# Kernel tuning notes

Hardware: AMD Instinct MI355X
Metric: run time of the kernel (lower is better)

The kernel has to match this reference:

```python
import jax, jax.numpy as jnp
import numpy as np

NPOINT, NSAMPLE, RADIUS, EPS = 128, 32, 0.4, 1e-5
C_IN, C_MID, C_OUT = 256, 256, 256


def setup_inputs() -> dict:
    key = jax.random.key(0)
    ks = jax.random.split(key, 6)
    B, N = 8, 16384
    xyz = jax.random.uniform(ks[0], (B, N, 3), dtype=jnp.float32)
    feats = jax.random.normal(ks[1], (B, N, C_IN), dtype=jnp.float32)
    # SharedMLP: Conv2d 1x1 (no bias, followed by BN) layers 259->256, 256->256
    w1 = jax.random.normal(ks[2], (C_MID, C_IN + 3), dtype=jnp.float32) * 0.05
    w2 = jax.random.normal(ks[3], (C_OUT, C_MID), dtype=jnp.float32) * 0.05
    gamma1 = jnp.ones((C_MID,), jnp.float32); beta1 = jnp.zeros((C_MID,), jnp.float32)
    mean1 = jnp.zeros((C_MID,), jnp.float32); var1 = jnp.ones((C_MID,), jnp.float32)
    gamma2 = jnp.ones((C_OUT,), jnp.float32); beta2 = jnp.zeros((C_OUT,), jnp.float32)
    mean2 = jnp.zeros((C_OUT,), jnp.float32); var2 = jnp.ones((C_OUT,), jnp.float32)
    return {"xyz": xyz, "proposal_features": feats,
            "w1": w1, "gamma1": gamma1, "beta1": beta1, "mean1": mean1, "var1": var1,
            "w2": w2, "gamma2": gamma2, "beta2": beta2, "mean2": mean2, "var2": var2}


def fps(xyz, npoint):
    # Farthest point sampling, CUDA-kernel-faithful: starts at index 0.
    B, N, _ = xyz.shape
    def step(carry, _):
        dist, far = carry
        centroid = jnp.take_along_axis(xyz, far[:, None, None], axis=1)  # [B,1,3]
        d = jnp.sum((xyz - centroid) ** 2, axis=-1)                      # [B,N]
        dist = jnp.minimum(dist, d)
        return (dist, jnp.argmax(dist, axis=-1).astype(jnp.int32)), far
    init = (jnp.full((B, N), 1e10, xyz.dtype), jnp.zeros((B,), jnp.int32))
    _, inds = jax.lax.scan(step, init, None, length=npoint)
    return inds.T  # [B, npoint]


def ball_query(xyz, new_xyz, radius, nsample):
    # First-nsample-in-order points within radius, padded with the first hit.
    B, N, _ = xyz.shape
    d2 = jnp.sum((new_xyz[:, :, None, :] - xyz[:, None, :, :]) ** 2, axis=-1)  # [B,S,N]
    keys = jnp.where(d2 < radius * radius, jnp.arange(N, dtype=jnp.int32), N)
    idx = -jax.lax.top_k(-keys, nsample)[0]  # smallest indices, ascending
    idx = jnp.where(idx < N, idx, idx[..., :1])  # pad invalid with first hit
    return jnp.clip(idx, 0, N - 1)


def gather_points(pts_bnc, idx):
    # pts_bnc [B,N,C], idx [B,S,K] -> [B,S,K,C]
    B, S, K = idx.shape
    flat = jnp.take_along_axis(pts_bnc, idx.reshape(B, S * K)[:, :, None], axis=1)
    return flat.reshape(B, S, K, pts_bnc.shape[-1])


def bn_relu(x, gamma, beta, mean, var):
    return jax.nn.relu((x - mean) * jax.lax.rsqrt(var + EPS) * gamma + beta)


def reference(xyz, proposal_features, w1, gamma1, beta1, mean1, var1,
              w2, gamma2, beta2, mean2, var2):
    # proposal_features arrives as [B, N, C]; torch module permutes to [B, C, N]
    # (we keep channels-last internally, equivalent math).
    inds = fps(xyz, NPOINT)                                   # [B,128]
    new_xyz = jnp.take_along_axis(xyz, inds[:, :, None], axis=1)  # [B,128,3]
    idx = ball_query(xyz, new_xyz, RADIUS, NSAMPLE)           # [B,128,32]
    g_xyz = gather_points(xyz, idx) - new_xyz[:, :, None, :]  # [B,128,32,3]
    g_feat = gather_points(proposal_features, idx)            # [B,128,32,256]
    x = jnp.concatenate([g_xyz, g_feat], axis=-1)             # [B,128,32,259]
    h = bn_relu(jnp.einsum('bskc,oc->bsko', x, w1), gamma1, beta1, mean1, var1)
    h = bn_relu(jnp.einsum('bskc,oc->bsko', h, w2), gamma2, beta2, mean2, var2)
    new_features = jnp.max(h, axis=2)                         # [B,128,256]
    return jnp.transpose(new_features, (0, 2, 1))             # [B,256,128]
```

## Files before the change

### kernel.cpp

```cpp
#include <hip/hip_runtime.h>
#include <hip/hip_bf16.h>
#include <cstdint>
#include <cstddef>

#define NB      8
#define NPTS    16384
#define NPOINT  128
#define NSAMPLE 32
#define CIN     256
#define CMID    256
#define COUT    256
#define KDIM    259
#define KPAD    288
#define XS_STRIDE 296
#define HS_STRIDE 264

typedef __attribute__((ext_vector_type(8))) short bf16x8;
typedef __attribute__((ext_vector_type(4))) float f32x4;
typedef __attribute__((ext_vector_type(2))) float f32x2;

__device__ __forceinline__ short f2bf(float f) {
  unsigned u = __float_as_uint(f);
  u += 0x7fffu + ((u >> 16) & 1u);
  return (short)(u >> 16);
}

template <int CTRL, int RMASK>
__device__ __forceinline__ unsigned long long dpp_umax_step(unsigned long long v) {
  int lo = (int)(unsigned)(v & 0xffffffffull);
  int hi = (int)(unsigned)(v >> 32);
  int nlo = __builtin_amdgcn_update_dpp(lo, lo, CTRL, RMASK, 0xf, false);
  int nhi = __builtin_amdgcn_update_dpp(hi, hi, CTRL, RMASK, 0xf, false);
  unsigned long long o = ((unsigned long long)(unsigned)nhi << 32) | (unsigned)nlo;
  return o > v ? o : v;
}

#define FPS_T 512
#define FPS_W (FPS_T / 64)
#define FPS_P (NPTS / FPS_T)
#define FPS_PH (FPS_P / 2)

__global__ __launch_bounds__(FPS_T) __attribute__((amdgpu_waves_per_eu(2, 2)))
void fps_kernel(const float* __restrict__ xyz, int* __restrict__ inds) {
#pragma clang fp contract(off)
  const int b = blockIdx.x;
  const int t = threadIdx.x;
  const int lane = t & 63, w = t >> 6;
  const float* xb = xyz + (size_t)b * NPTS * 3;

  f32x2 px[FPS_PH], py[FPS_PH], pz[FPS_PH], dv[FPS_PH];
#pragma unroll
  for (int i = 0; i < FPS_PH; ++i) {
    const int j0 = t + (2 * i) * FPS_T;
    const int j1 = j0 + FPS_T;
    px[i] = (f32x2){xb[j0 * 3 + 0], xb[j1 * 3 + 0]};
    py[i] = (f32x2){xb[j0 * 3 + 1], xb[j1 * 3 + 1]};
    pz[i] = (f32x2){xb[j0 * 3 + 2], xb[j1 * 3 + 2]};
    dv[i] = (f32x2){1e10f, 1e10f};
  }
#pragma unroll
  for (int i = 0; i < FPS_PH; ++i) {
    asm volatile("" : "+v"(px[i]), "+v"(py[i]), "+v"(pz[i]), "+v"(dv[i]));
  }

  __shared__ unsigned long long s_pack[2][FPS_W];
  __shared__ float swx[2][FPS_W], swy[2][FPS_W], swz[2][FPS_W];

  int far = 0;
  float cx = xb[0], cy = xb[1], cz = xb[2];

  for (int it = 0; it < NPOINT; ++it) {
    if (t == 0) inds[b * NPOINT + it] = far;
    const f32x2 vcx = {cx, cx}, vcy = {cy, cy}, vcz = {cz, cz};
    f32x2 best2 = {-1.0f, -1.0f};
#pragma unroll
    for (int i = 0; i < FPS_PH; ++i) {
      f32x2 dx = px[i] - vcx;
      f32x2 dy = py[i] - vcy;
      f32x2 dz = pz[i] - vcz;
      f32x2 d2 = (dx * dx + dy * dy) + dz * dz;
      f32x2 dm = {fminf(dv[i].x, d2.x), fminf(dv[i].y, d2.y)};
      dv[i] = dm;
      best2 = (f32x2){fmaxf(best2.x, dm.x), fmaxf(best2.y, dm.y)};
    }
    const float best = fmaxf(best2.x, best2.y);
    int sl = 0;
#pragma unroll
    for (int i = FPS_PH - 1; i >= 0; --i) {
      if (dv[i].y == best) sl = 2 * i + 1;
      if (dv[i].x == best) sl = 2 * i;
    }
    const int bi = t + (sl << 9);

    unsigned long long pk = ((unsigned long long)__float_as_uint(best) << 17)
                          | ((unsigned long long)(unsigned)(NPTS - 1 - bi) << 3)
                          | (unsigned long long)w;

    pk = dpp_umax_step<0x111, 0xf>(pk);
    pk = dpp_umax_step<0x112, 0xf>(pk);
    pk = dpp_umax_step<0x114, 0xf>(pk);
    pk = dpp_umax_step<0x118, 0xf>(pk);
    pk = dpp_umax_step<0x142, 0xa>(pk);
    pk = dpp_umax_step<0x143, 0xc>(pk);
    const unsigned wlo = (unsigned)__builtin_amdgcn_readlane((int)(unsigned)(pk & 0xffffffffull), 63);
    const unsigned whi = (unsigned)__builtin_amdgcn_readlane((int)(unsigned)(pk >> 32), 63);
    const unsigned long long wavepk = ((unsigned long long)whi << 32) | wlo;
    const int wbi = (NPTS - 1) - (int)((wavepk >> 3) & (unsigned long long)(NPTS - 1));

    const int slot = __builtin_amdgcn_readfirstlane(wbi >> 9);
    float bx = 0.f, by = 0.f, bz = 0.f;
#define CASE_SLOT(k) \
    case (2 * (k)):     bx = px[k].x; by = py[k].x; bz = pz[k].x; break; \
    case (2 * (k) + 1): bx = px[k].y; by = py[k].y; bz = pz[k].y; break;
    switch (slot) {
      CASE_SLOT(0)  CASE_SLOT(1)  CASE_SLOT(2)  CASE_SLOT(3)
      CASE_SLOT(4)  CASE_SLOT(5)  CASE_SLOT(6)  CASE_SLOT(7)
      CASE_SLOT(8)  CASE_SLOT(9)  CASE_SLOT(10) CASE_SLOT(11)
      CASE_SLOT(12) CASE_SLOT(13) CASE_SLOT(14) CASE_SLOT(15)
      default: break;
    }
#undef CASE_SLOT

    const int par = it & 1;
    if (lane == (wbi & 63)) {
      s_pack[par][w] = wavepk;
      swx[par][w] = bx; swy[par][w] = by; swz[par][w] = bz;
    }
    __syncthreads();
    unsigned long long pm = s_pack[par][lane & 7];
    pm = dpp_umax_step<0x124, 0xf>(pm);
    pm = dpp_umax_step<0x4E, 0xf>(pm);
    pm = dpp_umax_step<0xB1, 0xf>(pm);
    const int wi = (int)(pm & 7ull);
    far = (NPTS - 1) - (int)((pm >> 3) & (unsigned long long)(NPTS - 1));
    cx = swx[par][wi]; cy = swy[par][wi]; cz = swz[par][wi];
  }
}

__global__ __launch_bounds__(256) void ballq_kernel(const float* __restrict__ xyz,
                                                    const int* __restrict__ inds,
                                                    int* __restrict__ idx) {
  const int gw   = (blockIdx.x * 256 + threadIdx.x) >> 6;
  const int lane = threadIdx.x & 63;
  const int b = gw >> 7, s = gw & 127;
  const float* xb = xyz + (size_t)b * NPTS * 3;
  const int ind = inds[b * NPOINT + s];
  const float cx = xb[ind * 3 + 0], cy = xb[ind * 3 + 1], cz = xb[ind * 3 + 2];
  int* o = idx + gw * NSAMPLE;
  const float R2 = (float)(0.4 * 0.4);
  int total = 0;
  int first_hit = 0;
  bool have_first = false;
  for (int base = 0; base < NPTS && total < NSAMPLE; base += 64) {
    const int j = base + lane;
    float dx = __fsub_rn(xb[j * 3 + 0], cx);
    float dy = __fsub_rn(xb[j * 3 + 1], cy);
    float dz = __fsub_rn(xb[j * 3 + 2], cz);
    float d2 = __fadd_rn(__fadd_rn(__fmul_rn(dx, dx), __fmul_rn(dy, dy)), __fmul_rn(dz, dz));
    bool hit = d2 < R2;
    unsigned long long m = __ballot(hit);
    if (!have_first && m) { first_hit = base + (int)__builtin_ctzll(m); have_first = true; }
    int pos = total + (int)__popcll(m & ((1ull << lane) - 1ull));
    if (hit && pos < NSAMPLE) o[pos] = j;
    total += (int)__popcll(m);
  }
  for (int p = total + lane; p < NSAMPLE; p += 64) o[p] = first_hit;
}

__global__ __launch_bounds__(256) void prep_kernel(
    const float* __restrict__ w1, const float* __restrict__ g1, const float* __restrict__ be1,
    const float* __restrict__ m1, const float* __restrict__ v1,
    const float* __restrict__ w2, const float* __restrict__ g2, const float* __restrict__ be2,
    const float* __restrict__ m2, const float* __restrict__ v2,
    short* __restrict__ w1b, short* __restrict__ w2b,
    float* __restrict__ b1, float* __restrict__ b2) {
  int i = blockIdx.x * 256 + threadIdx.x;
  if (i < CMID * KPAD) {
    int oc = i / KPAD, c = i - oc * KPAD;
    float a = g1[oc] * rsqrtf(v1[oc] + 1e-5f);
    float val = (c < KDIM) ? w1[oc * KDIM + c] * a : 0.0f;
    w1b[i] = f2bf(val);
    if (c == 0) b1[oc] = be1[oc] - m1[oc] * a;
  }
  if (i < COUT * CMID) {
    int oc = i >> 8, c = i & 255;
    float a = g2[oc] * rsqrtf(v2[oc] + 1e-5f);
    w2b[i] = f2bf(w2[oc * CMID + c] * a);
    if (c == 0) b2[oc] = be2[oc] - m2[oc] * a;
  }
}

__global__ __launch_bounds__(256) void mlp_kernel(
    const float* __restrict__ xyz, const float* __restrict__ feats,
    const int* __restrict__ inds, const int* __restrict__ idx,
    const short* __restrict__ w1b, const short* __restrict__ w2b,
    const float* __restrict__ b1, const float* __restrict__ b2,
    float* __restrict__ out) {
  const int g   = blockIdx.x;
  const int bb  = g >> 7, s = g & 127;
  const int tid = threadIdx.x;
  const int wave = tid >> 6, lane = tid & 63;
  const int lrow = lane & 15, quad = lane >> 4;

  __shared__ short Xs[32 * XS_STRIDE];
  __shared__ short Hs[32 * HS_STRIDE];
  __shared__ int   sj[NSAMPLE];
  __shared__ float scen[3];

  if (tid < NSAMPLE) sj[tid] = idx[g * NSAMPLE + tid];
  if (tid < 3) {
    int ind = inds[bb * NPOINT + s];
    scen[tid] = xyz[((size_t)bb * NPTS + ind) * 3 + tid];
  }
  __syncthreads();

  for (int e = tid; e < 32 * KPAD; e += 256) {
    int r = e / KPAD, c = e - r * KPAD;
    int j = sj[r];
    float val;
    if (c < 3)          val = xyz[((size_t)bb * NPTS + j) * 3 + c] - scen[c];
    else if (c < KDIM)  val = feats[((size_t)bb * NPTS + j) * CIN + (c - 3)];
    else                val = 0.0f;
    Xs[r * XS_STRIDE + c] = f2bf(val);
  }
  __syncthreads();

  const int nw = wave * 64;
  f32x4 acc[4][2];
#pragma unroll
  for (int nt = 0; nt < 4; ++nt)
#pragma unroll
    for (int mt = 0; mt < 2; ++mt) acc[nt][mt] = (f32x4){0.f, 0.f, 0.f, 0.f};

  for (int ks = 0; ks < 9; ++ks) {
    const int ko = ks * 32 + quad * 8;
    bf16x8 a0 = *(const bf16x8*)(&Xs[lrow * XS_STRIDE + ko]);
    bf16x8 a1 = *(const bf16x8*)(&Xs[(lrow + 16) * XS_STRIDE + ko]);
#pragma unroll
    for (int nt = 0; nt < 4; ++nt) {
      const int oc = nw + nt * 16 + lrow;
      bf16x8 bf = *(const bf16x8*)(w1b + oc * KPAD + ko);
      acc[nt][0] = __builtin_amdgcn_mfma_f32_16x16x32_bf16(a0, bf, acc[nt][0], 0, 0, 0);
      acc[nt][1] = __builtin_amdgcn_mfma_f32_16x16x32_bf16(a1, bf, acc[nt][1], 0, 0, 0);
    }
  }

#pragma unroll
  for (int nt = 0; nt < 4; ++nt) {
    const int oc = nw + nt * 16 + lrow;
    const float bias = b1[oc];
#pragma unroll
    for (int mt = 0; mt < 2; ++mt) {
#pragma unroll
      for (int r = 0; r < 4; ++r) {
        int row = mt * 16 + quad * 4 + r;
        float h = fmaxf(acc[nt][mt][r] + bias, 0.0f);
        Hs[row * HS_STRIDE + oc] = f2bf(h);
      }
    }
  }
  __syncthreads();

#pragma unroll
  for (int nt = 0; nt < 4; ++nt)
#pragma unroll
    for (int mt = 0; mt < 2; ++mt) acc[nt][mt] = (f32x4){0.f, 0.f, 0.f, 0.f};

  for (int ks = 0; ks < 8; ++ks) {
    const int ko = ks * 32 + quad * 8;
    bf16x8 a0 = *(const bf16x8*)(&Hs[lrow * HS_STRIDE + ko]);
    bf16x8 a1 = *(const bf16x8*)(&Hs[(lrow + 16) * HS_STRIDE + ko]);
#pragma unroll
    for (int nt = 0; nt < 4; ++nt) {
      const int oc = nw + nt * 16 + lrow;
      bf16x8 bf = *(const bf16x8*)(w2b + oc * CMID + ko);
      acc[nt][0] = __builtin_amdgcn_mfma_f32_16x16x32_bf16(a0, bf, acc[nt][0], 0, 0, 0);
      acc[nt][1] = __builtin_amdgcn_mfma_f32_16x16x32_bf16(a1, bf, acc[nt][1], 0, 0, 0);
    }
  }

#pragma unroll
  for (int nt = 0; nt < 4; ++nt) {
    const int oc = nw + nt * 16 + lrow;
    const float bias = b2[oc];
    float v = -3.4e38f;
#pragma unroll
    for (int mt = 0; mt < 2; ++mt) {
      f32x4 a = acc[nt][mt];
      v = fmaxf(v, fmaxf(fmaxf(a[0], a[1]), fmaxf(a[2], a[3])));
    }
    v = fmaxf(v + bias, 0.0f);
    v = fmaxf(v, __shfl_xor(v, 16, 64));
    v = fmaxf(v, __shfl_xor(v, 32, 64));
    if (lane < 16) out[((size_t)bb * COUT + oc) * NPOINT + s] = v;
  }
}

extern "C" void kernel_launch(void* const* d_in, const int* in_sizes, int n_in,
                              void* d_out, int out_size, void* d_ws, size_t ws_size,
                              hipStream_t stream) {
  const float* xyz   = (const float*)d_in[0];
  const float* feats = (const float*)d_in[1];
  const float* w1    = (const float*)d_in[2];
  const float* g1    = (const float*)d_in[3];
  const float* be1   = (const float*)d_in[4];
  const float* m1    = (const float*)d_in[5];
  const float* v1    = (const float*)d_in[6];
  const float* w2    = (const float*)d_in[7];
  const float* g2    = (const float*)d_in[8];
  const float* be2   = (const float*)d_in[9];
  const float* m2    = (const float*)d_in[10];
  const float* v2    = (const float*)d_in[11];
  float* out = (float*)d_out;

  char* ws = (char*)d_ws;
  int*   inds = (int*)(ws);
  int*   idx  = (int*)(ws + 4096);
  short* w1b  = (short*)(ws + 135168);
  short* w2b  = (short*)(ws + 282624);
  float* b1   = (float*)(ws + 413696);
  float* b2   = (float*)(ws + 414720);

  prep_kernel<<<288, 256, 0, stream>>>(w1, g1, be1, m1, v1, w2, g2, be2, m2, v2,
                                       w1b, w2b, b1, b2);
  fps_kernel<<<NB, FPS_T, 0, stream>>>(xyz, inds);
  ballq_kernel<<<256, 256, 0, stream>>>(xyz, inds, idx);
  mlp_kernel<<<NB * NPOINT, 256, 0, stream>>>(xyz, feats, inds, idx, w1b, w2b, b1, b2, out);
}
```

Before: 456.4 us.

## Split farthest point sampling across four blocks per batch with global atomic sync

Each batch's farthest point sampling now runs on four workgroups, each owning a quarter of the points, so each thread holds fewer points and does less work per iteration. The per-block winners are merged every iteration through a global atomicMax on a packed distance/index key plus an arrival counter that the blocks spin on. The new centroid is then reloaded from global memory instead of being broadcast through shared memory. This adds a device-wide synchronisation round trip on each of the 128 iterations. The spin loop has a timeout, so correctness assumes all 32 workgroups are co-resident.

```diff
diff --git a/kernel.cpp b/kernel.cpp
--- a/kernel.cpp
+++ b/kernel.cpp
@@ -35,23 +35,30 @@
   return o > v ? o : v;
 }
 
-#define FPS_T 512
-#define FPS_W (FPS_T / 64)
-#define FPS_P (NPTS / FPS_T)
+#define FPS_K  4
+#define FPS_T  512
+#define FPS_W  (FPS_T / 64)
+#define FPS_PTS (NPTS / FPS_K)
+#define FPS_P  (FPS_PTS / FPS_T)
 #define FPS_PH (FPS_P / 2)
 
 __global__ __launch_bounds__(FPS_T) __attribute__((amdgpu_waves_per_eu(2, 2)))
-void fps_kernel(const float* __restrict__ xyz, int* __restrict__ inds) {
+void fps_kernel(const float* __restrict__ xyz, int* __restrict__ inds,
+                unsigned long long* __restrict__ slot, unsigned* __restrict__ cnt) {
 #pragma clang fp contract(off)
-  const int b = blockIdx.x;
+  const int bk = blockIdx.x;
+  const int b = bk >> 2, k = bk & 3;
   const int t = threadIdx.x;
   const int lane = t & 63, w = t >> 6;
   const float* xb = xyz + (size_t)b * NPTS * 3;
+  const int base = k * FPS_PTS;
+  unsigned long long* sl_b = slot + b * NPOINT;
+  unsigned* cn_b = cnt + b * NPOINT;
 
   f32x2 px[FPS_PH], py[FPS_PH], pz[FPS_PH], dv[FPS_PH];
 #pragma unroll
   for (int i = 0; i < FPS_PH; ++i) {
-    const int j0 = t + (2 * i) * FPS_T;
+    const int j0 = base + t + (2 * i) * FPS_T;
     const int j1 = j0 + FPS_T;
     px[i] = (f32x2){xb[j0 * 3 + 0], xb[j1 * 3 + 0]};
     py[i] = (f32x2){xb[j0 * 3 + 1], xb[j1 * 3 + 1]};
@@ -64,13 +71,12 @@
   }
 
   __shared__ unsigned long long s_pack[2][FPS_W];
-  __shared__ float swx[2][FPS_W], swy[2][FPS_W], swz[2][FPS_W];
 
   int far = 0;
   float cx = xb[0], cy = xb[1], cz = xb[2];
 
   for (int it = 0; it < NPOINT; ++it) {
-    if (t == 0) inds[b * NPOINT + it] = far;
+    if (k == 0 && t == 0) inds[b * NPOINT + it] = far;
     const f32x2 vcx = {cx, cx}, vcy = {cy, cy}, vcz = {cz, cz};
     f32x2 best2 = {-1.0f, -1.0f};
 #pragma unroll
@@ -90,11 +96,10 @@
       if (dv[i].y == best) sl = 2 * i + 1;
       if (dv[i].x == best) sl = 2 * i;
     }
-    const int bi = t + (sl << 9);
-
-    unsigned long long pk = ((unsigned long long)__float_as_uint(best) << 17)
-                          | ((unsigned long long)(unsigned)(NPTS - 1 - bi) << 3)
-                          | (unsigned long long)w;
+    const int bi = base + t + (sl << 9);
+
+    unsigned long long pk = ((unsigned long long)__float_as_uint(best) << 14)
+                          | (unsigned long long)(unsigned)(NPTS - 1 - bi);
 
     pk = dpp_umax_step<0x111, 0xf>(pk);
     pk = dpp_umax_step<0x112, 0xf>(pk);
@@ -105,35 +110,29 @@
     const unsigned wlo = (unsigned)__builtin_amdgcn_readlane((int)(unsigned)(pk & 0xffffffffull), 63);
     const unsigned whi = (unsigned)__builtin_amdgcn_readlane((int)(unsigned)(pk >> 32), 63);
     const unsigned long long wavepk = ((unsigned long long)whi << 32) | wlo;
-    const int wbi = (NPTS - 1) - (int)((wavepk >> 3) & (unsigned long long)(NPTS - 1));
-
-    const int slot = __builtin_amdgcn_readfirstlane(wbi >> 9);
-    float bx = 0.f, by = 0.f, bz = 0.f;
-#define CASE_SLOT(k) \
-    case (2 * (k)):     bx = px[k].x; by = py[k].x; bz = pz[k].x; break; \
-    case (2 * (k) + 1): bx = px[k].y; by = py[k].y; bz = pz[k].y; break;
-    switch (slot) {
-      CASE_SLOT(0)  CASE_SLOT(1)  CASE_SLOT(2)  CASE_SLOT(3)
-      CASE_SLOT(4)  CASE_SLOT(5)  CASE_SLOT(6)  CASE_SLOT(7)
-      CASE_SLOT(8)  CASE_SLOT(9)  CASE_SLOT(10) CASE_SLOT(11)
-      CASE_SLOT(12) CASE_SLOT(13) CASE_SLOT(14) CASE_SLOT(15)
-      default: break;
-    }
-#undef CASE_SLOT
 
     const int par = it & 1;
-    if (lane == (wbi & 63)) {
-      s_pack[par][w] = wavepk;
-      swx[par][w] = bx; swy[par][w] = by; swz[par][w] = bz;
-    }
+    if (lane == 0) s_pack[par][w] = wavepk;
     __syncthreads();
     unsigned long long pm = s_pack[par][lane & 7];
     pm = dpp_umax_step<0x124, 0xf>(pm);
     pm = dpp_umax_step<0x4E, 0xf>(pm);
     pm = dpp_umax_step<0xB1, 0xf>(pm);
-    const int wi = (int)(pm & 7ull);
-    far = (NPTS - 1) - (int)((pm >> 3) & (unsigned long long)(NPTS - 1));
-    cx = swx[par][wi]; cy = swy[par][wi]; cz = swz[par][wi];
+
+    if (t == 0) {
+      atomicMax(sl_b + it, pm);
+      __threadfence();
+      atomicAdd(cn_b + it, 1u);
+    }
+    unsigned spins = 0;
+    while (__hip_atomic_load(cn_b + it, __ATOMIC_ACQUIRE,
+                             __HIP_MEMORY_SCOPE_AGENT) < (unsigned)FPS_K) {
+      if (++spins > (1u << 20)) break;
+    }
+    const unsigned long long win = __hip_atomic_load(
+        sl_b + it, __ATOMIC_ACQUIRE, __HIP_MEMORY_SCOPE_AGENT);
+    far = (NPTS - 1) - (int)(win & (unsigned long long)(NPTS - 1));
+    cx = xb[far * 3 + 0]; cy = xb[far * 3 + 1]; cz = xb[far * 3 + 2];
   }
 }
 
@@ -173,8 +172,10 @@
     const float* __restrict__ w2, const float* __restrict__ g2, const float* __restrict__ be2,
     const float* __restrict__ m2, const float* __restrict__ v2,
     short* __restrict__ w1b, short* __restrict__ w2b,
-    float* __restrict__ b1, float* __restrict__ b2) {
+    float* __restrict__ b1, float* __restrict__ b2,
+    unsigned long long* __restrict__ slot, unsigned* __restrict__ cnt) {
   int i = blockIdx.x * 256 + threadIdx.x;
+  if (i < NB * NPOINT) { slot[i] = 0ull; cnt[i] = 0u; }
   if (i < CMID * KPAD) {
     int oc = i / KPAD, c = i - oc * KPAD;
     float a = g1[oc] * rsqrtf(v1[oc] + 1e-5f);
@@ -320,10 +321,12 @@
   short* w2b  = (short*)(ws + 282624);
   float* b1   = (float*)(ws + 413696);
   float* b2   = (float*)(ws + 414720);
+  unsigned long long* slot = (unsigned long long*)(ws + 415744);
+  unsigned* cnt = (unsigned*)(ws + 423936);
 
   prep_kernel<<<288, 256, 0, stream>>>(w1, g1, be1, m1, v1, w2, g2, be2, m2, v2,
-                                       w1b, w2b, b1, b2);
-  fps_kernel<<<NB, FPS_T, 0, stream>>>(xyz, inds);
+                                       w1b, w2b, b1, b2, slot, cnt);
+  fps_kernel<<<NB * FPS_K, FPS_T, 0, stream>>>(xyz, inds, slot, cnt);
   ballq_kernel<<<256, 256, 0, stream>>>(xyz, inds, idx);
   mlp_kernel<<<NB * NPOINT, 256, 0, stream>>>(xyz, feats, inds, idx, w1b, w2b, b1, b2, out);
 }
```

Result: slower. 1.188 ms (+160.3%).

## Fuse ball query into MLP kernel and vectorize feature gather with reordered weights

Applied to the files above, without the earlier changes.

Removes the separate ball-query kernel. Wave 0 of each MLP block now performs the radius search and writes the neighbor indices straight into shared memory, which saves one launch and a global round trip. The gather is restructured so features fill channels 0-255 with float4 loads and xyz offsets go to the tail, with the W1 columns permuted to match. Other waves sit idle during the search, and the search runs serially inside each block.

```diff
diff --git a/kernel.cpp b/kernel.cpp
--- a/kernel.cpp
+++ b/kernel.cpp
@@ -16,6 +16,7 @@
 #define HS_STRIDE 264
 
 typedef __attribute__((ext_vector_type(8))) short bf16x8;
+typedef __attribute__((ext_vector_type(4))) short s16x4;
 typedef __attribute__((ext_vector_type(4))) float f32x4;
 typedef __attribute__((ext_vector_type(2))) float f32x2;
 
@@ -137,36 +138,6 @@
   }
 }
 
-__global__ __launch_bounds__(256) void ballq_kernel(const float* __restrict__ xyz,
-                                                    const int* __restrict__ inds,
-                                                    int* __restrict__ idx) {
-  const int gw   = (blockIdx.x * 256 + threadIdx.x) >> 6;
-  const int lane = threadIdx.x & 63;
-  const int b = gw >> 7, s = gw & 127;
-  const float* xb = xyz + (size_t)b * NPTS * 3;
-  const int ind = inds[b * NPOINT + s];
-  const float cx = xb[ind * 3 + 0], cy = xb[ind * 3 + 1], cz = xb[ind * 3 + 2];
-  int* o = idx + gw * NSAMPLE;
-  const float R2 = (float)(0.4 * 0.4);
-  int total = 0;
-  int first_hit = 0;
-  bool have_first = false;
-  for (int base = 0; base < NPTS && total < NSAMPLE; base += 64) {
-    const int j = base + lane;
-    float dx = __fsub_rn(xb[j * 3 + 0], cx);
-    float dy = __fsub_rn(xb[j * 3 + 1], cy);
-    float dz = __fsub_rn(xb[j * 3 + 2], cz);
-    float d2 = __fadd_rn(__fadd_rn(__fmul_rn(dx, dx), __fmul_rn(dy, dy)), __fmul_rn(dz, dz));
-    bool hit = d2 < R2;
-    unsigned long long m = __ballot(hit);
-    if (!have_first && m) { first_hit = base + (int)__builtin_ctzll(m); have_first = true; }
-    int pos = total + (int)__popcll(m & ((1ull << lane) - 1ull));
-    if (hit && pos < NSAMPLE) o[pos] = j;
-    total += (int)__popcll(m);
-  }
-  for (int p = total + lane; p < NSAMPLE; p += 64) o[p] = first_hit;
-}
-
 __global__ __launch_bounds__(256) void prep_kernel(
     const float* __restrict__ w1, const float* __restrict__ g1, const float* __restrict__ be1,
     const float* __restrict__ m1, const float* __restrict__ v1,
@@ -176,11 +147,14 @@
     float* __restrict__ b1, float* __restrict__ b2) {
   int i = blockIdx.x * 256 + threadIdx.x;
   if (i < CMID * KPAD) {
-    int oc = i / KPAD, c = i - oc * KPAD;
+    int oc = i / KPAD, p = i - oc * KPAD;
     float a = g1[oc] * rsqrtf(v1[oc] + 1e-5f);
-    float val = (c < KDIM) ? w1[oc * KDIM + c] * a : 0.0f;
+    float val;
+    if (p < 256)      val = w1[oc * KDIM + 3 + p] * a;
+    else if (p < KDIM) val = w1[oc * KDIM + (p - 256)] * a;
+    else              val = 0.0f;
     w1b[i] = f2bf(val);
-    if (c == 0) b1[oc] = be1[oc] - m1[oc] * a;
+    if (p == 0) b1[oc] = be1[oc] - m1[oc] * a;
   }
   if (i < COUT * CMID) {
     int oc = i >> 8, c = i & 255;
@@ -192,7 +166,7 @@
 
 __global__ __launch_bounds__(256) void mlp_kernel(
     const float* __restrict__ xyz, const float* __restrict__ feats,
-    const int* __restrict__ inds, const int* __restrict__ idx,
+    const int* __restrict__ inds,
     const short* __restrict__ w1b, const short* __restrict__ w2b,
     const float* __restrict__ b1, const float* __restrict__ b2,
     float* __restrict__ out) {
@@ -205,23 +179,48 @@
   __shared__ short Xs[32 * XS_STRIDE];
   __shared__ short Hs[32 * HS_STRIDE];
   __shared__ int   sj[NSAMPLE];
-  __shared__ float scen[3];
-
-  if (tid < NSAMPLE) sj[tid] = idx[g * NSAMPLE + tid];
-  if (tid < 3) {
-    int ind = inds[bb * NPOINT + s];
-    scen[tid] = xyz[((size_t)bb * NPTS + ind) * 3 + tid];
+
+  const float* xb = xyz + (size_t)bb * NPTS * 3;
+  const int ind = inds[bb * NPOINT + s];
+  const float cx = xb[ind * 3 + 0], cy = xb[ind * 3 + 1], cz = xb[ind * 3 + 2];
+
+  if (wave == 0) {
+    const float R2 = (float)(0.4 * 0.4);
+    int total = 0;
+    int first_hit = 0;
+    bool have_first = false;
+    for (int base = 0; base < NPTS && total < NSAMPLE; base += 64) {
+      const int j = base + lane;
+      float dx = __fsub_rn(xb[j * 3 + 0], cx);
+      float dy = __fsub_rn(xb[j * 3 + 1], cy);
+      float dz = __fsub_rn(xb[j * 3 + 2], cz);
+      float d2 = __fadd_rn(__fadd_rn(__fmul_rn(dx, dx), __fmul_rn(dy, dy)), __fmul_rn(dz, dz));
+      bool hit = d2 < R2;
+      unsigned long long m = __ballot(hit);
+      if (!have_first && m) { first_hit = base + (int)__builtin_ctzll(m); have_first = true; }
+      int pos = total + (int)__popcll(m & ((1ull << lane) - 1ull));
+      if (hit && pos < NSAMPLE) sj[pos] = j;
+      total += (int)__popcll(m);
+    }
+    for (int p = total + lane; p < NSAMPLE; p += 64) sj[p] = first_hit;
   }
   __syncthreads();
 
-  for (int e = tid; e < 32 * KPAD; e += 256) {
-    int r = e / KPAD, c = e - r * KPAD;
-    int j = sj[r];
-    float val;
-    if (c < 3)          val = xyz[((size_t)bb * NPTS + j) * 3 + c] - scen[c];
-    else if (c < KDIM)  val = feats[((size_t)bb * NPTS + j) * CIN + (c - 3)];
-    else                val = 0.0f;
-    Xs[r * XS_STRIDE + c] = f2bf(val);
+  const float4* f4 = (const float4*)(feats + (size_t)bb * NPTS * CIN);
+  for (int u = tid; u < 32 * 64; u += 256) {
+    const int r = u >> 6, q = u & 63;
+    float4 v = f4[(size_t)sj[r] * 64 + q];
+    s16x4 pv = {f2bf(v.x), f2bf(v.y), f2bf(v.z), f2bf(v.w)};
+    *(s16x4*)(&Xs[r * XS_STRIDE + 4 * q]) = pv;
+  }
+  for (int u = tid; u < 32 * 32; u += 256) {
+    const int r = u >> 5, c = u & 31;
+    const int j = sj[r];
+    float val = 0.0f;
+    if (c == 0)      val = xb[j * 3 + 0] - cx;
+    else if (c == 1) val = xb[j * 3 + 1] - cy;
+    else if (c == 2) val = xb[j * 3 + 2] - cz;
+    Xs[r * XS_STRIDE + 256 + c] = f2bf(val);
   }
   __syncthreads();
 
@@ -315,7 +314,6 @@
 
   char* ws = (char*)d_ws;
   int*   inds = (int*)(ws);
-  int*   idx  = (int*)(ws + 4096);
   short* w1b  = (short*)(ws + 135168);
   short* w2b  = (short*)(ws + 282624);
   float* b1   = (float*)(ws + 413696);
@@ -324,6 +322,5 @@
   prep_kernel<<<288, 256, 0, stream>>>(w1, g1, be1, m1, v1, w2, g2, be2, m2, v2,
                                        w1b, w2b, b1, b2);
   fps_kernel<<<NB, FPS_T, 0, stream>>>(xyz, inds);
-  ballq_kernel<<<256, 256, 0, stream>>>(xyz, inds, idx);
-  mlp_kernel<<<NB * NPOINT, 256, 0, stream>>>(xyz, feats, inds, idx, w1b, w2b, b1, b2, out);
-}
+  mlp_kernel<<<NB * NPOINT, 256, 0, stream>>>(xyz, feats, inds, w1b, w2b, b1, b2, out);
+}
```

New measurement: 439.7 us. 3.6% less time.
